# Optimization experiments

Measured on AMD Instinct MI355X. Metric: run time of the kernel, lower is better.

## Reference

```python
import jax, jax.numpy as jnp
import numpy as np

TAU = 0.5

def setup_inputs() -> dict:
    key = jax.random.key(0)
    ks = jax.random.split(key, 20)
    B, D1, D2, E1, E2, U = 4096, 2000, 2000, 256, 256, 512
    M = E1 + E2
    s = lambda k, shp, scale=0.05: jax.random.normal(k, shp, dtype=jnp.float32) * scale
    return {
        "inputs": jax.random.normal(ks[0], (B, D1 + D2), dtype=jnp.float32),
        "h_tm1": jax.random.normal(ks[1], (B, U), dtype=jnp.float32),
        "crohis_tm": jax.random.normal(ks[2], (B, M), dtype=jnp.float32),
        "embed_weight_1": s(ks[3], (D1, E1)),
        "embed_weight_2": s(ks[4], (D2, E2)),
        "ca_1to2_w": s(ks[5], (E1, E1)),
        "ca_1to2_u": s(ks[6], (E2, E1)),
        "ca_1to2_v": s(ks[7], (E2, E1)),
        "ca_2to1_w": s(ks[8], (E2, E2)),
        "ca_2to1_u": s(ks[9], (E1, E2)),
        "ca_2to1_v": s(ks[10], (E1, E2)),
        "crohis_weight_w": s(ks[11], (M, U)),
        "crohis_bias": jnp.zeros((U,), jnp.float32),
        "crohis_decomp_weight": s(ks[12], (M, M)),
        "crohis_decomp_bias": jnp.zeros((M,), jnp.float32),
        "kernel": s(ks[13], (M, 3 * U)),
        "recurrent_kernel": s(ks[14], (U, 3 * U)),
        "bias": jnp.zeros((3 * U,), jnp.float32),
    }


def reference(inputs, h_tm1, crohis_tm,
              embed_weight_1, embed_weight_2,
              ca_1to2_w, ca_1to2_u, ca_1to2_v,
              ca_2to1_w, ca_2to1_u, ca_2to1_v,
              crohis_weight_w, crohis_bias,
              crohis_decomp_weight, crohis_decomp_bias,
              kernel, recurrent_kernel, bias):
    D1 = embed_weight_1.shape[0]
    U = recurrent_kernel.shape[0]
    # dual embedding lookups (dense multi-hot x embedding matrix)
    seqx1 = inputs[:, :D1]
    seqx2 = inputs[:, D1:]
    emb1 = seqx1 @ embed_weight_1   # [B, E1]
    emb2 = seqx2 @ embed_weight_2   # [B, E2]
    # cross-attention gates (softmax over feature axis, as K.softmax default)
    att12 = jax.nn.softmax(jnp.tanh(emb1 @ ca_1to2_w + emb2 @ ca_1to2_u) * (emb2 @ ca_1to2_v), axis=-1)
    att21 = jax.nn.softmax(jnp.tanh(emb2 @ ca_2to1_w + emb1 @ ca_2to1_u) * (emb1 @ ca_2to1_v), axis=-1)
    x = jnp.concatenate([emb1 * att12, emb2 * att21], axis=-1)  # [B, M]
    # cross-history decomposition modulating previous hidden state
    cro = jnp.tanh(crohis_tm @ crohis_decomp_weight + crohis_decomp_bias)
    h_prev = h_tm1 + jnp.tanh(cro @ crohis_weight_w + crohis_bias)
    # GRU (implementation=2, reset_after=False)
    mx = x @ kernel + bias                         # [B, 3U]
    x_z, x_r, x_h = mx[:, :U], mx[:, U:2 * U], mx[:, 2 * U:]
    mi = h_prev @ recurrent_kernel[:, :2 * U]      # [B, 2U]
    z = jax.nn.sigmoid(x_z + mi[:, :U])
    r = jax.nn.sigmoid(x_r + mi[:, U:])
    hh = jnp.tanh(x_h + (r * h_prev) @ recurrent_kernel[:, 2 * U:])
    h = z * h_prev + (1.0 - z) * hh
    # updated cross-history state (exponential moving average with tau)
    crohis_new = TAU * crohis_tm + (1.0 - TAU) * x
    return h, crohis_new
```

## Files before the change

### kernel.cpp

```cpp
#include <hip/hip_runtime.h>
#include <hip/hip_bf16.h>
#include <math.h>


#define TAU_F 0.5f

typedef __bf16 bf16x8 __attribute__((ext_vector_type(8)));
typedef __bf16 bf16x4 __attribute__((ext_vector_type(4)));
typedef float f32x4 __attribute__((ext_vector_type(4)));

__device__ __forceinline__ void gload16(const void* g, void* l) {
    __builtin_amdgcn_global_load_lds(
        (const __attribute__((address_space(1))) void*)g,
        (__attribute__((address_space(3))) void*)l, 16, 0, 0);
}

struct SubGemm {
    const void* A;
    int lda;
    int Kvalid;
    const __bf16* BT;
    int ldbt;
    float* C;
    int ldc;
    long long strideC;
    int Ksub;
    int nbx;
    int pairSplit;
    int pairAOff;
    int obf16;
};

template <bool AFP32>
__global__ __launch_bounds__(256) void gemm_dual(SubGemm g1, SubGemm g2, int blocks1)
{
    __shared__ __attribute__((aligned(16))) char lds[49152];

    const int tid = threadIdx.x, w = tid >> 6, l = tid & 63;

    const int gx = gridDim.x;
    const int nwg = gx * (int)gridDim.y;
    const int hw = (int)blockIdx.y * gx + (int)blockIdx.x;
    const int lg = (hw & 7) * (nwg >> 3) + (hw >> 3);
    const int bxl_lin = lg % gx;
    const int by = lg / gx;

    const bool second = bxl_lin >= blocks1;
    const SubGemm& g = second ? g2 : g1;
    const int bxl = second ? bxl_lin - blocks1 : bxl_lin;
    const int ct = bxl % g.nbx, spl = bxl / g.nbx;
    const int brow = by * 64, bcol = ct * 128;
    const int k_begin = spl * g.Ksub;
    const int nt = g.Ksub >> 5;
    const int aoff = (ct >= g.pairSplit) ? g.pairAOff : 0;

    const int sbr = w * 32 + (l >> 2);
    const int seg = (l & 3) * 8;

    const __bf16* Bg0 = g.BT + (size_t)(bcol + sbr) * g.ldbt + seg + k_begin;
    const __bf16* Bg1 = Bg0 + (size_t)16 * g.ldbt;

    f32x4 acc[2][4] = {};
    const int fr = l & 15, fk = (l >> 4) * 8;
    const int wr = (w >> 1) * 32, wc = (w & 1) * 64;
    const int kmax = (nt - 1) * 32;

    if constexpr (AFP32) {
        auto Af32 = (float (*)[64][32])lds;
        auto Bs   = (__bf16 (*)[128][32])(lds + 24576);

        const float* ArowBase = (const float*)g.A + aoff
                              + (size_t)(brow + w * 16 + (l >> 3)) * g.lda;
        const int colLane = (l & 7) * 4;
        const int kcl4 = g.Kvalid - 4;

#define ISSUE_A32(slot)                                                       \
        {                                                                     \
            const int _s = (slot);                                            \
            const int _k = (_s * 32 < kmax) ? _s * 32 : kmax;                 \
            const int _b = _s % 3;                                            \
            int c0 = k_begin + _k + colLane;                                  \
            c0 = c0 < kcl4 ? c0 : kcl4;                                       \
            gload16(ArowBase + c0,                 &Af32[_b][w * 16][0]);     \
            gload16(ArowBase + 8 * g.lda + c0,     &Af32[_b][w * 16 + 8][0]); \
            gload16(Bg0 + _k, &Bs[_b][w * 32][0]);                            \
            gload16(Bg1 + _k, &Bs[_b][w * 32 + 16][0]);                       \
        }

        ISSUE_A32(0) ISSUE_A32(1)

        for (int t = 0; t < nt; ++t) {
            asm volatile("s_waitcnt vmcnt(4)" ::: "memory");
            asm volatile("s_waitcnt lgkmcnt(0)" ::: "memory");
            __builtin_amdgcn_s_barrier();

            const int bi = t % 3;
            bf16x8 a[2]; bf16x8 b[4];
#pragma unroll
            for (int m = 0; m < 2; ++m) {
                f32x4 lo = *(const f32x4*)&Af32[bi][wr + m * 16 + fr][fk];
                f32x4 hi = *(const f32x4*)&Af32[bi][wr + m * 16 + fr][fk + 4];
#pragma unroll
                for (int z = 0; z < 4; ++z) { a[m][z] = (__bf16)lo[z]; a[m][4 + z] = (__bf16)hi[z]; }
            }
#pragma unroll
            for (int n = 0; n < 4; ++n) b[n] = *(const bf16x8*)&Bs[bi][wc + n * 16 + fr][fk];

            ISSUE_A32(t + 2)

#pragma unroll
            for (int m = 0; m < 2; ++m)
#pragma unroll
                for (int n = 0; n < 4; ++n)
                    acc[m][n] = __builtin_amdgcn_mfma_f32_16x16x32_bf16(a[m], b[n], acc[m][n], 0, 0, 0);
        }
#undef ISSUE_A32
    } else {
        auto As = (__bf16 (*)[64][32])lds;
        auto Bs = (__bf16 (*)[128][32])(lds + 16384);

        const int sar = w * 16 + (l >> 2);
        const __bf16* Ar = (const __bf16*)g.A + aoff
                         + (size_t)(brow + sar) * g.lda + seg + k_begin;

#define ISSUE_AB(slot)                                                        \
        {                                                                     \
            const int _s = (slot);                                            \
            const int _k = (_s * 32 < kmax) ? _s * 32 : kmax;                 \
            const int _b = _s & 3;                                            \
            gload16(Ar + _k,  &As[_b][w * 16][0]);                            \
            gload16(Bg0 + _k, &Bs[_b][w * 32][0]);                            \
            gload16(Bg1 + _k, &Bs[_b][w * 32 + 16][0]);                       \
        }

        ISSUE_AB(0) ISSUE_AB(1) ISSUE_AB(2)

        for (int t = 0; t < nt; ++t) {
            asm volatile("s_waitcnt vmcnt(6)" ::: "memory");
            asm volatile("s_waitcnt lgkmcnt(0)" ::: "memory");
            __builtin_amdgcn_s_barrier();

            const int bi = t & 3;
            bf16x8 a[2], b[4];
#pragma unroll
            for (int m = 0; m < 2; ++m) a[m] = *(const bf16x8*)&As[bi][wr + m * 16 + fr][fk];
#pragma unroll
            for (int n = 0; n < 4; ++n) b[n] = *(const bf16x8*)&Bs[bi][wc + n * 16 + fr][fk];

            ISSUE_AB(t + 3)

#pragma unroll
            for (int m = 0; m < 2; ++m)
#pragma unroll
                for (int n = 0; n < 4; ++n)
                    acc[m][n] = __builtin_amdgcn_mfma_f32_16x16x32_bf16(a[m], b[n], acc[m][n], 0, 0, 0);
        }
#undef ISSUE_AB
    }

    const int fq = (l >> 4) * 4;
    if (g.obf16) {
        __bf16* Cb = (__bf16*)g.C + (size_t)spl * g.strideC;
#pragma unroll
        for (int m = 0; m < 2; ++m)
#pragma unroll
            for (int n = 0; n < 4; ++n)
#pragma unroll
                for (int r = 0; r < 4; ++r) {
                    int row = brow + wr + m * 16 + fq + r;
                    int col = bcol + wc + n * 16 + fr;
                    Cb[(size_t)row * g.ldc + col] = (__bf16)acc[m][n][r];
                }
    } else {
        float* C = g.C + (size_t)spl * g.strideC;
#pragma unroll
        for (int m = 0; m < 2; ++m)
#pragma unroll
            for (int n = 0; n < 4; ++n)
#pragma unroll
                for (int r = 0; r < 4; ++r) {
                    int row = brow + wr + m * 16 + fq + r;
                    int col = bcol + wc + n * 16 + fr;
                    C[(size_t)row * g.ldc + col] = acc[m][n][r];
                }
    }
}

__global__ __launch_bounds__(256) void gemm_g8(
    const __bf16* __restrict__ A, const __bf16* __restrict__ BT,
    const float* __restrict__ mx, const float* __restrict__ mi2,
    const float* __restrict__ hprev, const float* __restrict__ bias,
    float* __restrict__ h)
{
    __shared__ __attribute__((aligned(16))) char lds[49152];

    const int tid = threadIdx.x, w = tid >> 6, l = tid & 63;

    const int gx = gridDim.x;
    const int nwg = gx * (int)gridDim.y;
    const int hw = (int)blockIdx.y * gx + (int)blockIdx.x;
    const int lg = (hw & 7) * (nwg >> 3) + (hw >> 3);
    const int ct = lg % gx;
    const int by = lg / gx;

    const int brow = by * 64, bcol = ct * 128;
    const int nt = 16;

    const int sbr = w * 32 + (l >> 2);
    const int seg = (l & 3) * 8;

    const __bf16* Bg0 = BT + (size_t)(bcol + sbr) * 512 + seg;
    const __bf16* Bg1 = Bg0 + (size_t)16 * 512;

    f32x4 acc[2][4] = {};
    const int fr = l & 15, fk = (l >> 4) * 8;
    const int wr = (w >> 1) * 32, wc = (w & 1) * 64;
    const int kmax = (nt - 1) * 32;

    auto As = (__bf16 (*)[64][32])lds;
    auto Bs = (__bf16 (*)[128][32])(lds + 16384);

    const int sar = w * 16 + (l >> 2);
    const __bf16* Ar = A + (size_t)(brow + sar) * 512 + seg;

#define ISSUE_G8(slot)                                                        \
    {                                                                         \
        const int _s = (slot);                                                \
        const int _k = (_s * 32 < kmax) ? _s * 32 : kmax;                     \
        const int _b = _s & 3;                                                \
        gload16(Ar + _k,  &As[_b][w * 16][0]);                                \
        gload16(Bg0 + _k, &Bs[_b][w * 32][0]);                                \
        gload16(Bg1 + _k, &Bs[_b][w * 32 + 16][0]);                           \
    }

    ISSUE_G8(0) ISSUE_G8(1) ISSUE_G8(2)

    for (int t = 0; t < nt; ++t) {
        asm volatile("s_waitcnt vmcnt(6)" ::: "memory");
        asm volatile("s_waitcnt lgkmcnt(0)" ::: "memory");
        __builtin_amdgcn_s_barrier();

        const int bi = t & 3;
        bf16x8 a[2], b[4];
#pragma unroll
        for (int m = 0; m < 2; ++m) a[m] = *(const bf16x8*)&As[bi][wr + m * 16 + fr][fk];
#pragma unroll
        for (int n = 0; n < 4; ++n) b[n] = *(const bf16x8*)&Bs[bi][wc + n * 16 + fr][fk];

        ISSUE_G8(t + 3)

#pragma unroll
        for (int m = 0; m < 2; ++m)
#pragma unroll
            for (int n = 0; n < 4; ++n)
                acc[m][n] = __builtin_amdgcn_mfma_f32_16x16x32_bf16(a[m], b[n], acc[m][n], 0, 0, 0);
    }
#undef ISSUE_G8

    const int fq = (l >> 4) * 4;
#pragma unroll
    for (int m = 0; m < 2; ++m)
#pragma unroll
        for (int n = 0; n < 4; ++n)
#pragma unroll
            for (int r = 0; r < 4; ++r) {
                int row = brow + wr + m * 16 + fq + r;
                int col = bcol + wc + n * 16 + fr;
                float xz = mx[(size_t)row * 1536 + col]        + bias[col];
                float xh = mx[(size_t)row * 1536 + 1024 + col] + bias[1024 + col];
                float mz = mi2[(size_t)row * 1024 + col];
                float hp = hprev[(size_t)row * 512 + col];
                float z  = 1.f / (1.f + expf(-(xz + mz)));
                float hh = tanhf(xh + acc[m][n][r]);
                h[(size_t)row * 512 + col] = z * hp + (1.f - z) * hh;
            }
}

__global__ __launch_bounds__(256) void prep_wT(
    const float* __restrict__ ew1, const float* __restrict__ ew2,
    const float* __restrict__ w12, const float* __restrict__ u12,
    const float* __restrict__ v12, const float* __restrict__ w21,
    const float* __restrict__ u21, const float* __restrict__ v21,
    const float* __restrict__ cd_w, const float* __restrict__ cw_w,
    const float* __restrict__ kern, const float* __restrict__ rkern,
    __bf16* __restrict__ WT, __bf16* __restrict__ WcatT,
    __bf16* __restrict__ cdT, __bf16* __restrict__ cwT,
    __bf16* __restrict__ kernT, __bf16* __restrict__ rkernT)
{
    __shared__ float tile[64][65];
    const int b = blockIdx.x, tid = threadIdx.x;
    const int tr = tid >> 6, tc = tid & 63;

    const float* src = nullptr;
    int ldsrc = 0, srow0 = 0, scol0 = 0, kvalid = 1 << 30;
    __bf16* dst; int ldd, n0, k0;
    bool zero = false;

    if (b < 256) {
        int q = b; n0 = (q >> 5) * 64; k0 = (q & 31) * 64;
        dst = WT; ldd = 2048; kvalid = 2000; ldsrc = 256; srow0 = k0;
        if (n0 < 256) { src = ew1; scol0 = n0; } else { src = ew2; scol0 = n0 - 256; }
    } else if (b < 384) {
        int q = b - 256; n0 = (q >> 3) * 64; k0 = (q & 7) * 64;
        dst = WcatT; ldd = 512; ldsrc = 256; srow0 = k0 & 255; scol0 = n0 & 255;
        int qn = n0 >> 8; bool khi = k0 >= 256;
        if (qn == 0)      src = khi ? u12 : w12;
        else if (qn == 1) src = khi ? w21 : u21;
        else if (qn == 2) { if (khi) src = v12; else zero = true; }
        else              { if (khi) zero = true; else src = v21; }
    } else if (b < 448) {
        int q = b - 384; n0 = (q >> 3) * 64; k0 = (q & 7) * 64;
        src = cd_w; ldsrc = 512; srow0 = k0; scol0 = n0; dst = cdT; ldd = 512;
    } else if (b < 512) {
        int q = b - 448; n0 = (q >> 3) * 64; k0 = (q & 7) * 64;
        src = cw_w; ldsrc = 512; srow0 = k0; scol0 = n0; dst = cwT; ldd = 512;
    } else if (b < 704) {
        int q = b - 512; n0 = (q >> 3) * 64; k0 = (q & 7) * 64;
        src = kern; ldsrc = 1536; srow0 = k0; scol0 = n0; dst = kernT; ldd = 512;
    } else {
        int q = b - 704; n0 = (q >> 3) * 64; k0 = (q & 7) * 64;
        src = rkern; ldsrc = 1536; srow0 = k0; scol0 = n0; dst = rkernT; ldd = 512;
    }

#pragma unroll
    for (int p = 0; p < 16; ++p) {
        int kr = p * 4 + tr;
        float v = 0.f;
        if (!zero && (srow0 + kr) < kvalid)
            v = src[(size_t)(srow0 + kr) * ldsrc + scol0 + tc];
        tile[kr][tc] = v;
    }
    __syncthreads();
#pragma unroll
    for (int p = 0; p < 16; ++p) {
        int nr = p * 4 + tr;
        dst[(size_t)(n0 + nr) * ldd + k0 + tc] = (__bf16)tile[tc][nr];
    }
}

__global__ __launch_bounds__(256) void reduce_A(
    const float* __restrict__ P12, const float* __restrict__ P4,
    const float* __restrict__ cd_b,
    __bf16* __restrict__ E, __bf16* __restrict__ cro)
{
    const int S = 1 << 21;
    int b = blockIdx.x;
    int i = (((b & 2047) * 256) + threadIdx.x) * 4;
    if (b < 2048) {
        f32x4 p0 = *(const f32x4*)(P12 + i);
        f32x4 p1 = *(const f32x4*)(P12 + S + i);
        __bf16 o[4];
#pragma unroll
        for (int j = 0; j < 4; ++j) o[j] = (__bf16)(p0[j] + p1[j]);
        *(bf16x4*)&E[i] = *(bf16x4*)o;
    } else {
        f32x4 p0 = *(const f32x4*)(P4 + i);
        int c = i & 511;
        __bf16 o[4];
#pragma unroll
        for (int j = 0; j < 4; ++j) o[j] = (__bf16)tanhf(p0[j] + cd_b[c + j]);
        *(bf16x4*)&cro[i] = *(bf16x4*)o;
    }
}

__global__ __launch_bounds__(256) void fuse1(
    const __bf16* __restrict__ T, const __bf16* __restrict__ E,
    const float* __restrict__ crohis,
    const float* __restrict__ P5,
    const float* __restrict__ h_tm1, const float* __restrict__ cw_b,
    __bf16* __restrict__ x, float* __restrict__ cro_out,
    float* __restrict__ hprev, __bf16* __restrict__ hprev_bf)
{
    __shared__ float s4[4];
    int b = blockIdx.x;
    int j = threadIdx.x;
    if (b < 4096) {
        const __bf16* t = T + (size_t)b * 1024;
        float s12 = tanhf((float)t[j])       * (float)t[512 + j];
        float s21 = tanhf((float)t[256 + j]) * (float)t[768 + j];
        float v = s12;
#pragma unroll
        for (int o = 32; o >= 1; o >>= 1) v = fmaxf(v, __shfl_xor(v, o, 64));
        __syncthreads(); if ((j & 63) == 0) s4[j >> 6] = v; __syncthreads();
        float m12 = fmaxf(fmaxf(s4[0], s4[1]), fmaxf(s4[2], s4[3]));
        float e12 = expf(s12 - m12);
        v = e12;
#pragma unroll
        for (int o = 32; o >= 1; o >>= 1) v += __shfl_xor(v, o, 64);
        __syncthreads(); if ((j & 63) == 0) s4[j >> 6] = v; __syncthreads();
        float sum12 = s4[0] + s4[1] + s4[2] + s4[3];
        v = s21;
#pragma unroll
        for (int o = 32; o >= 1; o >>= 1) v = fmaxf(v, __shfl_xor(v, o, 64));
        __syncthreads(); if ((j & 63) == 0) s4[j >> 6] = v; __syncthreads();
        float m21 = fmaxf(fmaxf(s4[0], s4[1]), fmaxf(s4[2], s4[3]));
        float e21 = expf(s21 - m21);
        v = e21;
#pragma unroll
        for (int o = 32; o >= 1; o >>= 1) v += __shfl_xor(v, o, 64);
        __syncthreads(); if ((j & 63) == 0) s4[j >> 6] = v; __syncthreads();
        float sum21 = s4[0] + s4[1] + s4[2] + s4[3];

        size_t b0 = (size_t)b * 512 + j, b1 = b0 + 256;
        float x1 = (float)E[b0] * (e12 / sum12);
        float x2 = (float)E[b1] * (e21 / sum21);
        x[b0] = (__bf16)x1;
        x[b1] = (__bf16)x2;
        cro_out[b0] = TAU_F * crohis[b0] + (1.f - TAU_F) * x1;
        cro_out[b1] = TAU_F * crohis[b1] + (1.f - TAU_F) * x2;
    } else {
        int i = ((b - 4096) * 256 + j) * 4;
        f32x4 p = *(const f32x4*)(P5 + i);
        f32x4 ht = *(const f32x4*)(h_tm1 + i);
        int c = i & 511;
        f32x4 o; __bf16 ob[4];
#pragma unroll
        for (int q = 0; q < 4; ++q) {
            float hv = ht[q] + tanhf(p[q] + cw_b[c + q]);
            o[q] = hv; ob[q] = (__bf16)hv;
        }
        *(f32x4*)(hprev + i) = o;
        *(bf16x4*)&hprev_bf[i] = *(bf16x4*)ob;
    }
}

__global__ __launch_bounds__(256) void gates_k(
    const float* __restrict__ mx, const float* __restrict__ mi2,
    const float* __restrict__ hprev, const float* __restrict__ bias,
    __bf16* __restrict__ rh)
{
    int i = (blockIdx.x * 256 + threadIdx.x) * 4;
    int row = i >> 9, c = i & 511;
    f32x4 a  = *(const f32x4*)(mx + (size_t)row * 1536 + 512 + c);
    f32x4 m  = *(const f32x4*)(mi2 + (size_t)row * 1024 + 512 + c);
    f32x4 hp = *(const f32x4*)(hprev + i);
    f32x4 bb = *(const f32x4*)(bias + 512 + c);
    __bf16 o[4];
#pragma unroll
    for (int q = 0; q < 4; ++q) {
        float r = 1.f / (1.f + expf(-(a[q] + bb[q] + m[q])));
        o[q] = (__bf16)(r * hp[q]);
    }
    *(bf16x4*)&rh[i] = *(bf16x4*)o;
}

extern "C" void kernel_launch(void* const* d_in, const int* in_sizes, int n_in,
                              void* d_out, int out_size, void* d_ws, size_t ws_size,
                              hipStream_t stream)
{
    (void)in_sizes; (void)n_in; (void)out_size; (void)ws_size;

    const float* inputs = (const float*)d_in[0];
    const float* h_tm1  = (const float*)d_in[1];
    const float* crohis = (const float*)d_in[2];
    const float* ew1    = (const float*)d_in[3];
    const float* ew2    = (const float*)d_in[4];
    const float* ca12w  = (const float*)d_in[5];
    const float* ca12u  = (const float*)d_in[6];
    const float* ca12v  = (const float*)d_in[7];
    const float* ca21w  = (const float*)d_in[8];
    const float* ca21u  = (const float*)d_in[9];
    const float* ca21v  = (const float*)d_in[10];
    const float* cw_w   = (const float*)d_in[11];
    const float* cw_b   = (const float*)d_in[12];
    const float* cd_w   = (const float*)d_in[13];
    const float* cd_b   = (const float*)d_in[14];
    const float* kern   = (const float*)d_in[15];
    const float* rkern  = (const float*)d_in[16];
    const float* bias   = (const float*)d_in[17];

    char* ws = (char*)d_ws;
    const size_t MB = 1 << 20;
    float*  P12      = (float*)(ws + 0);
    float*  P4       = (float*)(ws + 16 * MB);
    __bf16* T        = (__bf16*)(ws + 16 * MB);
    float*  P5       = (float*)(ws + 32 * MB);
    __bf16* x        = (__bf16*)(ws + 40 * MB);
    __bf16* rh       = (__bf16*)(ws + 40 * MB);
    __bf16* E        = (__bf16*)(ws + 48 * MB);
    __bf16* cro_bf   = (__bf16*)(ws + 52 * MB);
    float*  hprev    = (float*)(ws + 60 * MB);
    __bf16* hprev_bf = (__bf16*)(ws + 68 * MB);
    float*  mx       = (float*)(ws + 0);
    float*  mi2      = (float*)(ws + 24 * MB);
    __bf16* WT       = (__bf16*)(ws + 72 * MB);
    __bf16* WcatT    = (__bf16*)(ws + 74 * MB);
    __bf16* cdT      = (__bf16*)(ws + 75 * MB);
    __bf16* cwT      = (__bf16*)(ws + 75 * MB + 512 * 1024);
    __bf16* kernT    = (__bf16*)(ws + 76 * MB);
    __bf16* rkernT   = (__bf16*)(ws + 77 * MB + 512 * 1024);

    float* h_out   = (float*)d_out;
    float* cro_out = (float*)d_out + 2 * 1048576;

    const int BIG = 1 << 30;
    const long long S2 = 1ll << 21;

    prep_wT<<<896, 256, 0, stream>>>(ew1, ew2, ca12w, ca12u, ca12v, ca21w,
                                     ca21u, ca21v, cd_w, cw_w, kern, rkern,
                                     WT, WcatT, cdT, cwT, kernT, rkernT);

    SubGemm gA1 = { inputs, 4000, 2000, WT,  2048, P12, 512, S2, 1024, 4, 2, 2000, 0 };
    SubGemm gA2 = { crohis,  512,  512, cdT,  512, P4,  512, 0,   512, 4, BIG, 0, 0 };
    gemm_dual<true><<<dim3(12, 64), 256, 0, stream>>>(gA1, gA2, 8);

    reduce_A<<<4096, 256, 0, stream>>>(P12, P4, cd_b, E, cro_bf);

    SubGemm gB1 = { E,      512, 512, WcatT, 512, (float*)T, 1024, 0, 512, 8, BIG, 0, 1 };
    SubGemm gB2 = { cro_bf, 512, 512, cwT,   512, P5,        512,  0, 512, 4, BIG, 0, 0 };
    gemm_dual<false><<<dim3(12, 64), 256, 0, stream>>>(gB1, gB2, 8);

    fuse1<<<6144, 256, 0, stream>>>(T, E, crohis, P5, h_tm1, cw_b,
                                    x, cro_out, hprev, hprev_bf);

    SubGemm gC1 = { x,        512, 512, kernT,  512, mx,  1536, 0, 512, 12, BIG, 0, 0 };
    SubGemm gC2 = { hprev_bf, 512, 512, rkernT, 512, mi2, 1024, 0, 512, 8,  BIG, 0, 0 };
    gemm_dual<false><<<dim3(20, 64), 256, 0, stream>>>(gC1, gC2, 12);

    gates_k<<<2048, 256, 0, stream>>>(mx, mi2, hprev, bias, rh);

    gemm_g8<<<dim3(4, 64), 256, 0, stream>>>(
        rh, rkernT + (size_t)1024 * 512, mx, mi2, hprev, bias, h_out);
}
```

Measured before the change: 131.9 us.

## Use 64x64-tile fp32-A GEMM with 4-way split-K for the embedding stage

Replaces the first dual GEMM (embedding plus crohis-decomp, fp32 A converted to bf16 in LDS) with a new 64x64-tile kernel and 4-way split-K over the 2000-wide embedding dimension. The grid grows from 768 to 2560 workgroups to raise occupancy and parallelism on this stage. reduce_A now sums four partials instead of two, and the workspace layout is shuffled so P12 can hold four partial slices. The new kernel uses double buffering with an extra barrier instead of triple buffering, and the split adds more partial-sum traffic.

```diff
diff --git a/kernel.cpp b/kernel.cpp
--- a/kernel.cpp
+++ b/kernel.cpp
@@ -13,6 +13,113 @@
     __builtin_amdgcn_global_load_lds(
         (const __attribute__((address_space(1))) void*)g,
         (__attribute__((address_space(3))) void*)l, 16, 0, 0);
+}
+
+struct SubGemm64 {
+    const float* A;
+    int lda;
+    int Kvalid;
+    const __bf16* BT;
+    int ldbt;
+    float* C;
+    int ldc;
+    long long strideC;
+    int Ksub;
+    int nbx;
+    int pairSplit;
+    int pairAOff;
+};
+
+__global__ __launch_bounds__(256) void gemm64_dual(SubGemm64 g1, SubGemm64 g2, int blocks1)
+{
+    __shared__ __attribute__((aligned(16))) char lds[24576];
+    auto As32 = (float (*)[64][32])lds;
+    auto Bs   = (__bf16 (*)[64][32])(lds + 16384);
+
+    const int tid = threadIdx.x, w = tid >> 6, l = tid & 63;
+
+    const int gx = gridDim.x;
+    const int nwg = gx * (int)gridDim.y;
+    const int hw = (int)blockIdx.y * gx + (int)blockIdx.x;
+    const int lg = (hw & 7) * (nwg >> 3) + (hw >> 3);
+    const int bxl_lin = lg % gx;
+    const int by = lg / gx;
+
+    const bool second = bxl_lin >= blocks1;
+    const SubGemm64& g = second ? g2 : g1;
+    const int bxl = second ? bxl_lin - blocks1 : bxl_lin;
+    const int ct = bxl % g.nbx, spl = bxl / g.nbx;
+    const int brow = by * 64, bcol = ct * 64;
+    const int k_begin = spl * g.Ksub;
+    const int nt = g.Ksub >> 5;
+    const int aoff = (ct >= g.pairSplit) ? g.pairAOff : 0;
+
+    const float* Ar0 = g.A + aoff + (size_t)(brow + w * 16 + (l >> 3)) * g.lda;
+    const float* Ar8 = Ar0 + (size_t)8 * g.lda;
+    const int colLane = (l & 7) * 4;
+    const int kcl4 = g.Kvalid - 4;
+    const __bf16* Bg = g.BT + (size_t)(bcol + w * 16 + (l >> 2)) * g.ldbt
+                     + (l & 3) * 8 + k_begin;
+
+    f32x4 acc[2][2] = {};
+    const int fr = l & 15, fk = (l >> 4) * 8;
+    const int wr = (w >> 1) * 32, wc = (w & 1) * 32;
+    const int kmax = (nt - 1) * 32;
+
+#define ISS64(slot)                                                          \
+    {                                                                        \
+        const int _s = (slot);                                               \
+        const int _k = (_s * 32 < kmax) ? _s * 32 : kmax;                    \
+        const int _b = _s & 1;                                               \
+        int c0 = k_begin + _k + colLane;                                     \
+        c0 = c0 < kcl4 ? c0 : kcl4;                                          \
+        gload16(Ar0 + c0, &As32[_b][w * 16][0]);                             \
+        gload16(Ar8 + c0, &As32[_b][w * 16 + 8][0]);                         \
+        gload16(Bg + _k,  &Bs[_b][w * 16][0]);                               \
+    }
+
+    ISS64(0) ISS64(1)
+
+    for (int t = 0; t < nt; ++t) {
+        asm volatile("s_waitcnt vmcnt(3)" ::: "memory");
+        asm volatile("s_waitcnt lgkmcnt(0)" ::: "memory");
+        asm volatile("s_barrier" ::: "memory");
+
+        const int bi = t & 1;
+        bf16x8 a[2], b[2];
+#pragma unroll
+        for (int m = 0; m < 2; ++m) {
+            f32x4 lo = *(const f32x4*)&As32[bi][wr + m * 16 + fr][fk];
+            f32x4 hi = *(const f32x4*)&As32[bi][wr + m * 16 + fr][fk + 4];
+#pragma unroll
+            for (int z = 0; z < 4; ++z) { a[m][z] = (__bf16)lo[z]; a[m][4 + z] = (__bf16)hi[z]; }
+        }
+#pragma unroll
+        for (int n = 0; n < 2; ++n) b[n] = *(const bf16x8*)&Bs[bi][wc + n * 16 + fr][fk];
+
+#pragma unroll
+        for (int m = 0; m < 2; ++m)
+#pragma unroll
+            for (int n = 0; n < 2; ++n)
+                acc[m][n] = __builtin_amdgcn_mfma_f32_16x16x32_bf16(a[m], b[n], acc[m][n], 0, 0, 0);
+
+        asm volatile("s_barrier" ::: "memory");
+        ISS64(t + 2)
+    }
+#undef ISS64
+
+    float* C = g.C + (size_t)spl * g.strideC;
+    const int fq = (l >> 4) * 4;
+#pragma unroll
+    for (int m = 0; m < 2; ++m)
+#pragma unroll
+        for (int n = 0; n < 2; ++n)
+#pragma unroll
+            for (int r = 0; r < 4; ++r) {
+                int row = brow + wr + m * 16 + fq + r;
+                int col = bcol + wc + n * 16 + fr;
+                C[(size_t)row * g.ldc + col] = acc[m][n][r];
+            }
 }
 
 struct SubGemm {
@@ -31,7 +138,6 @@
     int obf16;
 };
 
-template <bool AFP32>
 __global__ __launch_bounds__(256) void gemm_dual(SubGemm g1, SubGemm g2, int blocks1)
 {
     __shared__ __attribute__((aligned(16))) char lds[49152];
@@ -65,98 +171,46 @@
     const int wr = (w >> 1) * 32, wc = (w & 1) * 64;
     const int kmax = (nt - 1) * 32;
 
-    if constexpr (AFP32) {
-        auto Af32 = (float (*)[64][32])lds;
-        auto Bs   = (__bf16 (*)[128][32])(lds + 24576);
-
-        const float* ArowBase = (const float*)g.A + aoff
-                              + (size_t)(brow + w * 16 + (l >> 3)) * g.lda;
-        const int colLane = (l & 7) * 4;
-        const int kcl4 = g.Kvalid - 4;
-
-#define ISSUE_A32(slot)                                                       \
-        {                                                                     \
-            const int _s = (slot);                                            \
-            const int _k = (_s * 32 < kmax) ? _s * 32 : kmax;                 \
-            const int _b = _s % 3;                                            \
-            int c0 = k_begin + _k + colLane;                                  \
-            c0 = c0 < kcl4 ? c0 : kcl4;                                       \
-            gload16(ArowBase + c0,                 &Af32[_b][w * 16][0]);     \
-            gload16(ArowBase + 8 * g.lda + c0,     &Af32[_b][w * 16 + 8][0]); \
-            gload16(Bg0 + _k, &Bs[_b][w * 32][0]);                            \
-            gload16(Bg1 + _k, &Bs[_b][w * 32 + 16][0]);                       \
-        }
-
-        ISSUE_A32(0) ISSUE_A32(1)
-
-        for (int t = 0; t < nt; ++t) {
-            asm volatile("s_waitcnt vmcnt(4)" ::: "memory");
-            asm volatile("s_waitcnt lgkmcnt(0)" ::: "memory");
-            __builtin_amdgcn_s_barrier();
-
-            const int bi = t % 3;
-            bf16x8 a[2]; bf16x8 b[4];
-#pragma unroll
-            for (int m = 0; m < 2; ++m) {
-                f32x4 lo = *(const f32x4*)&Af32[bi][wr + m * 16 + fr][fk];
-                f32x4 hi = *(const f32x4*)&Af32[bi][wr + m * 16 + fr][fk + 4];
-#pragma unroll
-                for (int z = 0; z < 4; ++z) { a[m][z] = (__bf16)lo[z]; a[m][4 + z] = (__bf16)hi[z]; }
-            }
-#pragma unroll
-            for (int n = 0; n < 4; ++n) b[n] = *(const bf16x8*)&Bs[bi][wc + n * 16 + fr][fk];
-
-            ISSUE_A32(t + 2)
-
-#pragma unroll
-            for (int m = 0; m < 2; ++m)
-#pragma unroll
-                for (int n = 0; n < 4; ++n)
-                    acc[m][n] = __builtin_amdgcn_mfma_f32_16x16x32_bf16(a[m], b[n], acc[m][n], 0, 0, 0);
-        }
-#undef ISSUE_A32
-    } else {
-        auto As = (__bf16 (*)[64][32])lds;
-        auto Bs = (__bf16 (*)[128][32])(lds + 16384);
-
-        const int sar = w * 16 + (l >> 2);
-        const __bf16* Ar = (const __bf16*)g.A + aoff
-                         + (size_t)(brow + sar) * g.lda + seg + k_begin;
+    auto As = (__bf16 (*)[64][32])lds;
+    auto Bs = (__bf16 (*)[128][32])(lds + 16384);
+
+    const int sar = w * 16 + (l >> 2);
+    const __bf16* Ar = (const __bf16*)g.A + aoff
+                     + (size_t)(brow + sar) * g.lda + seg + k_begin;
 
 #define ISSUE_AB(slot)                                                        \
-        {                                                                     \
-            const int _s = (slot);                                            \
-            const int _k = (_s * 32 < kmax) ? _s * 32 : kmax;                 \
-            const int _b = _s & 3;                                            \
-            gload16(Ar + _k,  &As[_b][w * 16][0]);                            \
-            gload16(Bg0 + _k, &Bs[_b][w * 32][0]);                            \
-            gload16(Bg1 + _k, &Bs[_b][w * 32 + 16][0]);                       \
-        }
-
-        ISSUE_AB(0) ISSUE_AB(1) ISSUE_AB(2)
-
-        for (int t = 0; t < nt; ++t) {
-            asm volatile("s_waitcnt vmcnt(6)" ::: "memory");
-            asm volatile("s_waitcnt lgkmcnt(0)" ::: "memory");
-            __builtin_amdgcn_s_barrier();
-
-            const int bi = t & 3;
-            bf16x8 a[2], b[4];
-#pragma unroll
-            for (int m = 0; m < 2; ++m) a[m] = *(const bf16x8*)&As[bi][wr + m * 16 + fr][fk];
-#pragma unroll
-            for (int n = 0; n < 4; ++n) b[n] = *(const bf16x8*)&Bs[bi][wc + n * 16 + fr][fk];
-
-            ISSUE_AB(t + 3)
-
-#pragma unroll
-            for (int m = 0; m < 2; ++m)
-#pragma unroll
-                for (int n = 0; n < 4; ++n)
-                    acc[m][n] = __builtin_amdgcn_mfma_f32_16x16x32_bf16(a[m], b[n], acc[m][n], 0, 0, 0);
-        }
+    {                                                                         \
+        const int _s = (slot);                                                \
+        const int _k = (_s * 32 < kmax) ? _s * 32 : kmax;                     \
+        const int _b = _s & 3;                                                \
+        gload16(Ar + _k,  &As[_b][w * 16][0]);                                \
+        gload16(Bg0 + _k, &Bs[_b][w * 32][0]);                                \
+        gload16(Bg1 + _k, &Bs[_b][w * 32 + 16][0]);                           \
+    }
+
+    ISSUE_AB(0) ISSUE_AB(1) ISSUE_AB(2)
+
+    for (int t = 0; t < nt; ++t) {
+        asm volatile("s_waitcnt vmcnt(6)" ::: "memory");
+        asm volatile("s_waitcnt lgkmcnt(0)" ::: "memory");
+        __builtin_amdgcn_s_barrier();
+
+        const int bi = t & 3;
+        bf16x8 a[2], b[4];
+#pragma unroll
+        for (int m = 0; m < 2; ++m) a[m] = *(const bf16x8*)&As[bi][wr + m * 16 + fr][fk];
+#pragma unroll
+        for (int n = 0; n < 4; ++n) b[n] = *(const bf16x8*)&Bs[bi][wc + n * 16 + fr][fk];
+
+        ISSUE_AB(t + 3)
+
+#pragma unroll
+        for (int m = 0; m < 2; ++m)
+#pragma unroll
+            for (int n = 0; n < 4; ++n)
+                acc[m][n] = __builtin_amdgcn_mfma_f32_16x16x32_bf16(a[m], b[n], acc[m][n], 0, 0, 0);
+    }
 #undef ISSUE_AB
-    }
 
     const int fq = (l >> 4) * 4;
     if (g.obf16) {
@@ -349,9 +403,11 @@
     if (b < 2048) {
         f32x4 p0 = *(const f32x4*)(P12 + i);
         f32x4 p1 = *(const f32x4*)(P12 + S + i);
+        f32x4 p2 = *(const f32x4*)(P12 + 2 * S + i);
+        f32x4 p3 = *(const f32x4*)(P12 + 3 * S + i);
         __bf16 o[4];
 #pragma unroll
-        for (int j = 0; j < 4; ++j) o[j] = (__bf16)(p0[j] + p1[j]);
+        for (int j = 0; j < 4; ++j) o[j] = (__bf16)((p0[j] + p1[j]) + (p2[j] + p3[j]));
         *(bf16x4*)&E[i] = *(bf16x4*)o;
     } else {
         f32x4 p0 = *(const f32x4*)(P4 + i);
@@ -472,17 +528,17 @@
     char* ws = (char*)d_ws;
     const size_t MB = 1 << 20;
     float*  P12      = (float*)(ws + 0);
-    float*  P4       = (float*)(ws + 16 * MB);
-    __bf16* T        = (__bf16*)(ws + 16 * MB);
-    float*  P5       = (float*)(ws + 32 * MB);
-    __bf16* x        = (__bf16*)(ws + 40 * MB);
-    __bf16* rh       = (__bf16*)(ws + 40 * MB);
-    __bf16* E        = (__bf16*)(ws + 48 * MB);
-    __bf16* cro_bf   = (__bf16*)(ws + 52 * MB);
+    float*  mx       = (float*)(ws + 0);
+    float*  P4       = (float*)(ws + 32 * MB);
+    __bf16* T        = (__bf16*)(ws + 32 * MB);
+    float*  mi2      = (float*)(ws + 24 * MB);
+    float*  P5       = (float*)(ws + 40 * MB);
+    __bf16* x        = (__bf16*)(ws + 48 * MB);
+    __bf16* rh       = (__bf16*)(ws + 48 * MB);
+    __bf16* E        = (__bf16*)(ws + 52 * MB);
+    __bf16* cro_bf   = (__bf16*)(ws + 56 * MB);
     float*  hprev    = (float*)(ws + 60 * MB);
     __bf16* hprev_bf = (__bf16*)(ws + 68 * MB);
-    float*  mx       = (float*)(ws + 0);
-    float*  mi2      = (float*)(ws + 24 * MB);
     __bf16* WT       = (__bf16*)(ws + 72 * MB);
     __bf16* WcatT    = (__bf16*)(ws + 74 * MB);
     __bf16* cdT      = (__bf16*)(ws + 75 * MB);
@@ -500,22 +556,22 @@
                                      ca21u, ca21v, cd_w, cw_w, kern, rkern,
                                      WT, WcatT, cdT, cwT, kernT, rkernT);
 
-    SubGemm gA1 = { inputs, 4000, 2000, WT,  2048, P12, 512, S2, 1024, 4, 2, 2000, 0 };
-    SubGemm gA2 = { crohis,  512,  512, cdT,  512, P4,  512, 0,   512, 4, BIG, 0, 0 };
-    gemm_dual<true><<<dim3(12, 64), 256, 0, stream>>>(gA1, gA2, 8);
+    SubGemm64 gA1 = { inputs, 4000, 2000, WT,  2048, P12, 512, S2, 512, 8, 4,   2000 };
+    SubGemm64 gA2 = { crohis,  512,  512, cdT,  512, P4,  512, 0,  512, 8, BIG, 0 };
+    gemm64_dual<<<dim3(40, 64), 256, 0, stream>>>(gA1, gA2, 32);
 
     reduce_A<<<4096, 256, 0, stream>>>(P12, P4, cd_b, E, cro_bf);
 
     SubGemm gB1 = { E,      512, 512, WcatT, 512, (float*)T, 1024, 0, 512, 8, BIG, 0, 1 };
     SubGemm gB2 = { cro_bf, 512, 512, cwT,   512, P5,        512,  0, 512, 4, BIG, 0, 0 };
-    gemm_dual<false><<<dim3(12, 64), 256, 0, stream>>>(gB1, gB2, 8);
+    gemm_dual<<<dim3(12, 64), 256, 0, stream>>>(gB1, gB2, 8);
 
     fuse1<<<6144, 256, 0, stream>>>(T, E, crohis, P5, h_tm1, cw_b,
                                     x, cro_out, hprev, hprev_bf);
 
     SubGemm gC1 = { x,        512, 512, kernT,  512, mx,  1536, 0, 512, 12, BIG, 0, 0 };
     SubGemm gC2 = { hprev_bf, 512, 512, rkernT, 512, mi2, 1024, 0, 512, 8,  BIG, 0, 0 };
-    gemm_dual<false><<<dim3(20, 64), 256, 0, stream>>>(gC1, gC2, 12);
+    gemm_dual<<<dim3(20, 64), 256, 0, stream>>>(gC1, gC2, 12);
 
     gates_k<<<2048, 256, 0, stream>>>(mx, mi2, hprev, bias, rh);
 
```

Result: slower. 143.7 us (+9.0%).

## Load fp32 A operand directly into registers instead of staging through LDS

Applied to the files above, without the earlier changes.

In the fp32-A GEMM path, A tiles are now read from global memory straight into registers, double-buffered in two sets and converted to bf16 in place, instead of being copied into LDS with async loads and read back. Only B is staged in LDS, now with a 4-slot ring, which cuts LDS use for this variant from 48KB to 32KB. The aim is to remove the LDS round trip for A and to allow more resident workgroups. In exchange it uses more VGPRs, makes wait-count accounting harder (vmcnt changed to 6), and the loop assumes an even tile count. The per-lane global reads are also less coalesced.

```diff
diff --git a/kernel.cpp b/kernel.cpp
--- a/kernel.cpp
+++ b/kernel.cpp
@@ -34,7 +34,7 @@
 template <bool AFP32>
 __global__ __launch_bounds__(256) void gemm_dual(SubGemm g1, SubGemm g2, int blocks1)
 {
-    __shared__ __attribute__((aligned(16))) char lds[49152];
+    __shared__ __attribute__((aligned(16))) char lds[AFP32 ? 32768 : 49152];
 
     const int tid = threadIdx.x, w = tid >> 6, l = tid & 63;
 
@@ -66,55 +66,66 @@
     const int kmax = (nt - 1) * 32;
 
     if constexpr (AFP32) {
-        auto Af32 = (float (*)[64][32])lds;
-        auto Bs   = (__bf16 (*)[128][32])(lds + 24576);
-
-        const float* ArowBase = (const float*)g.A + aoff
-                              + (size_t)(brow + w * 16 + (l >> 3)) * g.lda;
-        const int colLane = (l & 7) * 4;
-        const int kcl4 = g.Kvalid - 4;
-
-#define ISSUE_A32(slot)                                                       \
+        auto Bs = (__bf16 (*)[128][32])lds;
+
+        const float* Ar0 = (const float*)g.A + aoff + (size_t)(brow + wr + fr) * g.lda;
+        const float* Ar1 = Ar0 + (size_t)16 * g.lda;
+        const int kcl = g.Kvalid - 8;
+
+#define ALOAD(d0, d1, d2, d3, slot)                                           \
+        {                                                                     \
+            const int _k = ((slot) * 32 < kmax) ? (slot) * 32 : kmax;         \
+            int c = k_begin + _k + fk;                                        \
+            c = c < kcl ? c : kcl;                                            \
+            d0 = *(const f32x4*)(Ar0 + c);                                    \
+            d1 = *(const f32x4*)(Ar0 + c + 4);                                \
+            d2 = *(const f32x4*)(Ar1 + c);                                    \
+            d3 = *(const f32x4*)(Ar1 + c + 4);                                \
+        }
+#define BLOAD(slot)                                                           \
         {                                                                     \
             const int _s = (slot);                                            \
             const int _k = (_s * 32 < kmax) ? _s * 32 : kmax;                 \
-            const int _b = _s % 3;                                            \
-            int c0 = k_begin + _k + colLane;                                  \
-            c0 = c0 < kcl4 ? c0 : kcl4;                                       \
-            gload16(ArowBase + c0,                 &Af32[_b][w * 16][0]);     \
-            gload16(ArowBase + 8 * g.lda + c0,     &Af32[_b][w * 16 + 8][0]); \
+            const int _b = _s & 3;                                            \
             gload16(Bg0 + _k, &Bs[_b][w * 32][0]);                            \
             gload16(Bg1 + _k, &Bs[_b][w * 32 + 16][0]);                       \
         }
-
-        ISSUE_A32(0) ISSUE_A32(1)
-
-        for (int t = 0; t < nt; ++t) {
-            asm volatile("s_waitcnt vmcnt(4)" ::: "memory");
-            asm volatile("s_waitcnt lgkmcnt(0)" ::: "memory");
-            __builtin_amdgcn_s_barrier();
-
-            const int bi = t % 3;
-            bf16x8 a[2]; bf16x8 b[4];
-#pragma unroll
-            for (int m = 0; m < 2; ++m) {
-                f32x4 lo = *(const f32x4*)&Af32[bi][wr + m * 16 + fr][fk];
-                f32x4 hi = *(const f32x4*)&Af32[bi][wr + m * 16 + fr][fk + 4];
-#pragma unroll
-                for (int z = 0; z < 4; ++z) { a[m][z] = (__bf16)lo[z]; a[m][4 + z] = (__bf16)hi[z]; }
-            }
-#pragma unroll
-            for (int n = 0; n < 4; ++n) b[n] = *(const bf16x8*)&Bs[bi][wc + n * 16 + fr][fk];
-
-            ISSUE_A32(t + 2)
-
-#pragma unroll
-            for (int m = 0; m < 2; ++m)
-#pragma unroll
-                for (int n = 0; n < 4; ++n)
-                    acc[m][n] = __builtin_amdgcn_mfma_f32_16x16x32_bf16(a[m], b[n], acc[m][n], 0, 0, 0);
-        }
-#undef ISSUE_A32
+#define ASTEP(t_, s0, s1, s2, s3)                                             \
+        {                                                                     \
+            asm volatile("s_waitcnt vmcnt(6)" ::: "memory");                  \
+            asm volatile("s_waitcnt lgkmcnt(0)" ::: "memory");                \
+            __builtin_amdgcn_s_barrier();                                     \
+            const int _bi = (t_) & 3;                                         \
+            bf16x8 a[2], b[4];                                                \
+            _Pragma("unroll")                                                 \
+            for (int z = 0; z < 4; ++z) {                                     \
+                a[0][z] = (__bf16)s0[z]; a[0][4 + z] = (__bf16)s1[z];         \
+                a[1][z] = (__bf16)s2[z]; a[1][4 + z] = (__bf16)s3[z];         \
+            }                                                                 \
+            _Pragma("unroll")                                                 \
+            for (int n = 0; n < 4; ++n)                                       \
+                b[n] = *(const bf16x8*)&Bs[_bi][wc + n * 16 + fr][fk];        \
+            ALOAD(s0, s1, s2, s3, (t_) + 2)                                   \
+            BLOAD((t_) + 2)                                                   \
+            _Pragma("unroll")                                                 \
+            for (int m = 0; m < 2; ++m)                                       \
+                _Pragma("unroll")                                             \
+                for (int n = 0; n < 4; ++n)                                   \
+                    acc[m][n] = __builtin_amdgcn_mfma_f32_16x16x32_bf16(      \
+                        a[m], b[n], acc[m][n], 0, 0, 0);                      \
+        }
+
+        f32x4 p0, p1, p2, p3, q0, q1, q2, q3;
+        ALOAD(p0, p1, p2, p3, 0) BLOAD(0)
+        ALOAD(q0, q1, q2, q3, 1) BLOAD(1)
+
+        for (int t = 0; t < nt; t += 2) {
+            ASTEP(t,     p0, p1, p2, p3)
+            ASTEP(t + 1, q0, q1, q2, q3)
+        }
+#undef ASTEP
+#undef BLOAD
+#undef ALOAD
     } else {
         auto As = (__bf16 (*)[64][32])lds;
         auto Bs = (__bf16 (*)[128][32])(lds + 16384);
```

New measurement: 155.4 us. +17.8%, slower.
